# Kernel tuning notes

Measured on AMD Instinct MI355X. Metric: run time of the kernel, lower is better.

The kernel has to match this reference:

```python
import jax, jax.numpy as jnp
import numpy as np
import math

B, C, MX, MY, MZ = 4, 64, 32, 32, 32
N_ATOM, EMB, N_HEAD = 64, 128, 8
HEAD = C // N_HEAD


def setup_inputs() -> dict:
    key = jax.random.key(0)
    ks = jax.random.split(key, 12)
    s = 0.05
    return {
        "x": jax.random.normal(ks[0], (B, C, MX, MY, MZ), jnp.float32),
        "mol_embed": jax.random.normal(ks[1], (B, N_ATOM, EMB), jnp.float32),
        "batch_nodes": jax.random.randint(ks[2], (B,), 1, N_ATOM + 1),  # >=1 valid atom
        "Wq": jax.random.normal(ks[3], (C, C), jnp.float32) * s,
        "bq": jnp.zeros((C,), jnp.float32),
        "Wk": jax.random.normal(ks[4], (C, EMB), jnp.float32) * s,
        "bk": jnp.zeros((C,), jnp.float32),
        "Wv": jax.random.normal(ks[5], (C, EMB), jnp.float32) * s,
        "bv": jnp.zeros((C,), jnp.float32),
        "Wo": jax.random.normal(ks[6], (C, C), jnp.float32) * s,
        "bo": jnp.zeros((C,), jnp.float32),
        "Wc": jax.random.normal(ks[7], (C, C, 3, 3, 3), jnp.float32) * s,
        "bc": jnp.zeros((C,), jnp.float32),
    }


def reference(x, mol_embed, batch_nodes, Wq, bq, Wk, bk, Wv, bv, Wo, bo, Wc, bc):
    b, c, mx, my, mz = x.shape
    m_voxel = mx * my * mz
    n_atom = mol_embed.shape[1]
    x_in = x

    # [b, m_voxel, c] voxel tokens
    xt = x.reshape(b, c, m_voxel).transpose(0, 2, 1)
    q = (xt @ Wq.T + bq).reshape(b, m_voxel, N_HEAD, HEAD)
    k = (mol_embed @ Wk.T + bk).reshape(b, n_atom, N_HEAD, HEAD)
    v = (mol_embed @ Wv.T + bv).reshape(b, n_atom, N_HEAD, HEAD)

    att = jnp.einsum('bqhd,bkhd->bhqk', q, k) / math.sqrt(HEAD)
    # ragged per-batch masking: atoms >= batch_nodes[i] are invalid
    valid = jnp.arange(n_atom)[None, :] < batch_nodes[:, None]  # [b, n_atom]
    att = jnp.where(valid[:, None, None, :], att, -jnp.inf)
    att = jax.nn.softmax(att, axis=-1)

    o = jnp.einsum('bhqk,bkhd->bqhd', att, v).reshape(b, m_voxel, c)
    o = jax.nn.relu(o @ Wo.T + bo)
    o = o.transpose(0, 2, 1).reshape(b, c, mx, my, mz)

    # conv3d k=3 with circular padding
    op = jnp.pad(o, ((0, 0), (0, 0), (1, 1), (1, 1), (1, 1)), mode='wrap')
    conv = jax.lax.conv_general_dilated(
        op, Wc, window_strides=(1, 1, 1), padding='VALID',
        dimension_numbers=('NCDHW', 'OIDHW', 'NCDHW'))
    conv = conv + bc[None, :, None, None, None]
    return jax.nn.relu(conv) + x_in
```

## Files before the change

### kernel.cpp

```cpp
#include <hip/hip_runtime.h>
#include <hip/hip_bf16.h>

#define B_    4
#define C_    64
#define MVOX  32768
#define NATOM 64
#define EMB_  128

typedef __attribute__((ext_vector_type(8)))  __bf16 bf16x8;
typedef __attribute__((ext_vector_type(4)))  float  f32x4;
typedef __attribute__((ext_vector_type(16))) float  f32x16;
typedef __attribute__((ext_vector_type(8)))  unsigned short ushort8;

typedef __attribute__((address_space(1))) const unsigned int gas_u32;
typedef __attribute__((address_space(3))) unsigned int las_u32;

static __device__ __forceinline__ unsigned short bf16u(float f) {
  __hip_bfloat16 h = __float2bfloat16(f);
  return *(unsigned short*)&h;
}

__global__ __launch_bounds__(256) void wprep_kernel(
    const float* __restrict__ Wc, const float* __restrict__ Wq,
    const float* __restrict__ Wo, const float* __restrict__ Wk,
    const float* __restrict__ Wv,
    __hip_bfloat16* __restrict__ Wt4, __hip_bfloat16* __restrict__ Wqb,
    __hip_bfloat16* __restrict__ Wob, __hip_bfloat16* __restrict__ Wkb,
    __hip_bfloat16* __restrict__ Wvb) {
  const int i = blockIdx.x * 256 + threadIdx.x;
  if (i < 110592) {
    const int tap = i >> 12;
    const int coh = (i >> 11) & 1;
    const int ks  = (i >> 9) & 3;
    const int l   = (i >> 3) & 63;
    const int j   = i & 7;
    const int co  = coh * 32 + (l & 31);
    const int ci  = ks * 16 + ((l >> 5) << 3) + j;
    Wt4[i] = __float2bfloat16(Wc[(co * C_ + ci) * 27 + tap]);
  } else if (i < 114688) {
    const int i2 = i - 110592;
    const int nf = (i2 >> 10) & 3;
    const int kk = (i2 >> 9) & 1;
    const int l  = (i2 >> 3) & 63;
    const int j  = i2 & 7;
    const int co = nf * 16 + (l & 15);
    const int ci = kk * 32 + ((l >> 4) << 3) + j;
    Wqb[i2] = __float2bfloat16(Wq[co * C_ + ci] * 0.3535533905932738f);
  } else if (i < 118784) {
    const int i3 = i - 114688;
    const int nf = (i3 >> 10) & 3;
    const int kk = (i3 >> 9) & 1;
    const int l  = (i3 >> 3) & 63;
    const int j  = i3 & 7;
    const int co = nf * 16 + (l & 15);
    const int ci = kk * 32 + ((l >> 4) << 3) + j;
    Wob[i3] = __float2bfloat16(Wo[co * C_ + ci]);
  } else if (i < 135168) {
    const int i4 = (i - 118784) & 8191;
    const bool is_v = (i - 118784) >= 8192;
    const int ch = i4 >> 12;
    const int kk = (i4 >> 9) & 7;
    const int l  = (i4 >> 3) & 63;
    const int j  = i4 & 7;
    const int c  = ch * 32 + (l & 31);
    const int e  = kk * 16 + ((l >> 5) << 3) + j;
    const float v = (is_v ? Wv : Wk)[c * EMB_ + e];
    (is_v ? Wvb : Wkb)[i4] = __float2bfloat16(v);
  }
}

__global__ __launch_bounds__(256) void kv_kernel(
    const float* __restrict__ mol,
    const __hip_bfloat16* __restrict__ Wkb, const float* __restrict__ bk,
    const __hip_bfloat16* __restrict__ Wvb, const float* __restrict__ bv,
    unsigned short* __restrict__ kfb, unsigned short* __restrict__ vfb) {
  __shared__ float smol[NATOM][132];
  __shared__ float res[2][NATOM][68];

  const int b    = blockIdx.x;
  const int tid  = threadIdx.x;
  const int lane = tid & 63;
  const int w    = tid >> 6;
  const int kvw  = w >> 1;
  const int ah   = w & 1;

  for (int i = tid; i < 2048; i += 256) {
    const int a = i >> 4, cb = (i & 15) * 8;
    const f32x4 v0 = *(const f32x4*)&mol[(size_t)(b * NATOM + a) * EMB_ + cb];
    const f32x4 v1 = *(const f32x4*)&mol[(size_t)(b * NATOM + a) * EMB_ + cb + 4];
    *(f32x4*)&smol[a][cb]     = v0;
    *(f32x4*)&smol[a][cb + 4] = v1;
  }
  __syncthreads();

  const __hip_bfloat16* Wb   = kvw ? Wvb : Wkb;
  const float*          bias = kvw ? bv : bk;

  f32x16 acc[2];
  #pragma unroll
  for (int ch = 0; ch < 2; ++ch)
    #pragma unroll
    for (int r = 0; r < 16; ++r) acc[ch][r] = 0.f;

  const int a = ah * 32 + (lane & 31);
  #pragma unroll
  for (int kk = 0; kk < 8; ++kk) {
    const int e0 = kk * 16 + ((lane >> 5) << 3);
    ushort8 au;
    #pragma unroll
    for (int j = 0; j < 8; ++j) au[j] = bf16u(smol[a][e0 + j]);
    const bf16x8 af = __builtin_bit_cast(bf16x8, au);
    #pragma unroll
    for (int ch = 0; ch < 2; ++ch) {
      const bf16x8 bf = *(const bf16x8*)(Wb + (((ch * 8 + kk) << 6) + lane) * 8);
      acc[ch] = __builtin_amdgcn_mfma_f32_32x32x16_bf16(af, bf, acc[ch], 0, 0, 0);
    }
  }

  #pragma unroll
  for (int ch = 0; ch < 2; ++ch) {
    const int c = ch * 32 + (lane & 31);
    const float bb = bias[c];
    #pragma unroll
    for (int r = 0; r < 16; ++r) {
      const int ar = ah * 32 + (r & 3) + 8 * (r >> 2) + 4 * (lane >> 5);
      res[kvw][ar][c] = acc[ch][r] + bb;
    }
  }
  __syncthreads();

  #pragma unroll
  for (int t = 0; t < 8; ++t) {
    const int idx = t * 256 + tid;
    const int h = idx >> 8, aa = (idx >> 6) & 3, ln = idx & 63;
    const int qd = ln >> 4, l15 = ln & 15;
    ushort8 au;
    if (qd == 0) {
      #pragma unroll
      for (int j = 0; j < 8; ++j) au[j] = bf16u(res[0][aa * 16 + l15][h * 8 + j]);
    } else {
      #pragma unroll
      for (int j = 0; j < 8; ++j) au[j] = 0;
    }
    *(ushort8*)(kfb + (size_t)(((b * 8 + h) * 4 + aa) * 64 + ln) * 8) = au;
  }
  #pragma unroll
  for (int t = 0; t < 4; ++t) {
    const int idx = t * 256 + tid;
    const int h = idx >> 7, s = (idx >> 6) & 1, ln = idx & 63;
    const int qd = ln >> 4, l15 = ln & 15;
    ushort8 au;
    #pragma unroll
    for (int j = 0; j < 8; ++j) {
      const int atom = (2 * s + (j >> 2)) * 16 + qd * 4 + (j & 3);
      au[j] = bf16u(res[1][atom][h * 8 + (l15 & 7)]);
    }
    *(ushort8*)(vfb + (size_t)(((b * 8 + h) * 2 + s) * 64 + ln) * 8) = au;
  }
}

__global__ __launch_bounds__(512, 4) void attn_kernel(
    const float* __restrict__ x,
    const unsigned short* __restrict__ kfb, const unsigned short* __restrict__ vfb,
    const int* __restrict__ batch_nodes,
    const __hip_bfloat16* __restrict__ Wqb, const float* __restrict__ bq,
    const __hip_bfloat16* __restrict__ Wob, const float* __restrict__ bo,
    __hip_bfloat16* __restrict__ omid) {
  __shared__ float buf[64 * C_];

  const int b    = blockIdx.y;
  const int m0   = blockIdx.x * 64;
  const int tid  = threadIdx.x;
  const int lane = tid & 63;
  const int w    = __builtin_amdgcn_readfirstlane(tid >> 6);
  const int h    = w;
  const int quad = lane >> 4;
  const int l15  = lane & 15;
  const int vq   = w & 3;
  const int cq   = w >> 2;

  bf16x8 kf[4], vf[2];
  #pragma unroll
  for (int a = 0; a < 4; ++a)
    kf[a] = __builtin_bit_cast(bf16x8,
        *(const ushort8*)(kfb + (size_t)(((b * 8 + h) * 4 + a) * 64 + lane) * 8));
  #pragma unroll
  for (int s = 0; s < 2; ++s)
    vf[s] = __builtin_bit_cast(bf16x8,
        *(const ushort8*)(vfb + (size_t)(((b * 8 + h) * 2 + s) * 64 + lane) * 8));

  #pragma unroll
  for (int j = 0; j < 2; ++j) {
    const int cidx = w * 2 + j;
    const int c  = cidx * 4 + (lane >> 4);
    const int v4 = (lane & 15) * 4;
    const float* gsrc = x + (size_t)(b * C_ + c) * MVOX + m0 + v4;
    __builtin_amdgcn_global_load_lds((gas_u32*)gsrc,
                                     (las_u32*)&buf[cidx * 256], 16, 0, 0);
  }
  __syncthreads();

  f32x4 qacc[2];
  {
    bf16x8 af[2];
    #pragma unroll
    for (int kk = 0; kk < 2; ++kk) {
      ushort8 au;
      #pragma unroll
      for (int j = 0; j < 8; ++j)
        au[j] = bf16u(buf[(kk * 32 + quad * 8 + j) * 64 + vq * 16 + l15]);
      af[kk] = __builtin_bit_cast(bf16x8, au);
    }
    #pragma unroll
    for (int nf2 = 0; nf2 < 2; ++nf2) {
      const int nf = cq * 2 + nf2;
      const float bqv = bq[nf * 16 + l15] * 0.3535533905932738f;
      qacc[nf2] = {bqv, bqv, bqv, bqv};
      #pragma unroll
      for (int kk = 0; kk < 2; ++kk) {
        const bf16x8 bf = *(const bf16x8*)(Wqb + (((nf * 2 + kk) << 6) + lane) * 8);
        qacc[nf2] = __builtin_amdgcn_mfma_f32_16x16x32_bf16(af[kk], bf, qacc[nf2], 0, 0, 0);
      }
    }
  }
  __syncthreads();

  unsigned short* qb = (unsigned short*)buf;
  #pragma unroll
  for (int nf2 = 0; nf2 < 2; ++nf2) {
    const int co = (cq * 2 + nf2) * 16 + l15;
    #pragma unroll
    for (int r = 0; r < 4; ++r) {
      const int vr = vq * 16 + quad * 4 + r;
      qb[vr * 64 + (((co >> 3) ^ (vr & 7)) << 3) + (co & 7)] = bf16u(qacc[nf2][r]);
    }
  }
  __syncthreads();

  const int nv = batch_nodes[b];
  unsigned short* ob = (unsigned short*)buf + 4096;

  f32x4 oacc[4];
  #pragma unroll
  for (int v = 0; v < 4; ++v)
    #pragma unroll
    for (int r = 0; r < 4; ++r) oacc[v][r] = 0.f;

  const f32x4 zero4 = {0.f, 0.f, 0.f, 0.f};
  #pragma unroll
  for (int v = 0; v < 4; ++v) {
    const int qrow = v * 16 + l15;
    const bf16x8 qf = __builtin_bit_cast(bf16x8,
        *(const ushort8*)&qb[qrow * 64 + ((h ^ (qrow & 7)) << 3)]);

    f32x4 st[4];
    #pragma unroll
    for (int a = 0; a < 4; ++a)
      st[a] = __builtin_amdgcn_mfma_f32_16x16x32_bf16(kf[a], qf, zero4, 0, 0, 0);

    float m = -1e30f;
    #pragma unroll
    for (int a = 0; a < 4; ++a)
      #pragma unroll
      for (int r = 0; r < 4; ++r) {
        const int atom = a * 16 + quad * 4 + r;
        const float val = (atom < nv) ? st[a][r] : -1e30f;
        st[a][r] = val;
        m = fmaxf(m, val);
      }
    m = fmaxf(m, __shfl_xor(m, 16, 64));
    m = fmaxf(m, __shfl_xor(m, 32, 64));
    float ssum = 0.f;
    #pragma unroll
    for (int a = 0; a < 4; ++a)
      #pragma unroll
      for (int r = 0; r < 4; ++r) {
        const float p = __expf(st[a][r] - m);
        st[a][r] = p;
        ssum += p;
      }
    ssum += __shfl_xor(ssum, 16, 64);
    ssum += __shfl_xor(ssum, 32, 64);
    const float inv = 1.f / ssum;

    #pragma unroll
    for (int s = 0; s < 2; ++s) {
      ushort8 pu;
      #pragma unroll
      for (int j = 0; j < 8; ++j)
        pu[j] = bf16u(st[2 * s + (j >> 2)][j & 3] * inv);
      const bf16x8 pa = __builtin_bit_cast(bf16x8, pu);
      oacc[v] = __builtin_amdgcn_mfma_f32_16x16x32_bf16(pa, vf[s], oacc[v], 0, 0, 0);
    }
  }

  if (l15 < 8) {
    #pragma unroll
    for (int v = 0; v < 4; ++v)
      #pragma unroll
      for (int r = 0; r < 4; ++r) {
        const int vxr = v * 16 + quad * 4 + r;
        ob[vxr * 64 + ((h ^ (vxr & 7)) << 3) + l15] = bf16u(oacc[v][r]);
      }
  }
  __syncthreads();

  {
    bf16x8 af[2];
    #pragma unroll
    for (int kk = 0; kk < 2; ++kk) {
      const int row = vq * 16 + l15;
      af[kk] = __builtin_bit_cast(bf16x8,
          *(const ushort8*)&ob[row * 64 + (((kk * 4 + quad) ^ (row & 7)) << 3)]);
    }
    f32x4 oac[2];
    #pragma unroll
    for (int nf2 = 0; nf2 < 2; ++nf2) {
      const int nf = cq * 2 + nf2;
      const float bov = bo[nf * 16 + l15];
      oac[nf2] = {bov, bov, bov, bov};
      #pragma unroll
      for (int kk = 0; kk < 2; ++kk) {
        const bf16x8 bf = *(const bf16x8*)(Wob + (((nf * 2 + kk) << 6) + lane) * 8);
        oac[nf2] = __builtin_amdgcn_mfma_f32_16x16x32_bf16(af[kk], bf, oac[nf2], 0, 0, 0);
      }
    }
    __syncthreads();
    unsigned short* osb = (unsigned short*)buf;
    #pragma unroll
    for (int nf2 = 0; nf2 < 2; ++nf2) {
      const int co = (cq * 2 + nf2) * 16 + l15;
      #pragma unroll
      for (int r = 0; r < 4; ++r) {
        const int vr = vq * 16 + quad * 4 + r;
        osb[vr * 64 + (((co >> 3) ^ (vr & 7)) << 3) + (co & 7)] =
            bf16u(fmaxf(oac[nf2][r], 0.f));
      }
    }
  }
  __syncthreads();

  *(ushort8*)(omid + (size_t)(b * MVOX + m0) * C_ + tid * 8) =
      *(const ushort8*)&((unsigned short*)buf)[tid * 8];
}

#define LOADB(dst, DX, DY, DZ)                                              \
  {                                                                         \
    const int zp_ = ((lane & 31) + (DZ) + 31) & 31;                         \
    const int sw_ = zp_ & 7;                                                \
    const int hl_ = (lpx + (DX)) * 4 + (lpy + (DY));                        \
    _Pragma("unroll")                                                       \
    for (int ks_ = 0; ks_ < 4; ++ks_) {                                     \
      const int phys_ = (ks_ * 2 + (lane >> 5)) ^ sw_;                      \
      (dst)[ks_] = *(const bf16x8*)&halo[((hl_ * 32 + zp_) * 8 + phys_) * 8]; \
    }                                                                       \
  }

#define LOADW(T2)                                                           \
  _Pragma("unroll")                                                         \
  for (int f_ = 0; f_ < 8; ++f_)                                            \
    wf[(T2) % 3][f_] = *(const bf16x8*)(                                    \
        Wt4 + ((((T2) * 2 + (f_ >> 2)) * 4 + (f_ & 3)) << 9) + lane * 8);

#define DOMFMA(src, T)                                                      \
  _Pragma("unroll")                                                         \
  for (int ks_ = 0; ks_ < 4; ++ks_)                                         \
    _Pragma("unroll")                                                       \
    for (int ch_ = 0; ch_ < 2; ++ch_)                                       \
      acc[ch_] = __builtin_amdgcn_mfma_f32_32x32x16_bf16(                   \
          wf[(T) % 3][ch_ * 4 + ks_], (src)[ks_], acc[ch_], 0, 0, 0);

__global__ __launch_bounds__(256, 2) void conv_kernel(
    const __hip_bfloat16* __restrict__ omid,
    const __hip_bfloat16* __restrict__ Wt4,
    const float* __restrict__ bc,
    const float* __restrict__ xin,
    float* __restrict__ out) {
  __shared__ __hip_bfloat16 halo[512 * 64];

  const int b    = blockIdx.y;
  const int x0   = (blockIdx.x >> 4) * 2;
  const int y0   = (blockIdx.x & 15) * 2;
  const int tid  = threadIdx.x;
  const int lane = tid & 63;
  const int w    = tid >> 6;
  const int lpx  = w >> 1;
  const int lpy  = w & 1;

  {
    const __hip_bfloat16* src = omid + (size_t)b * MVOX * C_;
    #pragma unroll
    for (int n = 0; n < 16; ++n) {
      const int chunk = w * 16 + n;
      const int li = chunk >> 2;
      const int zb = (chunk & 3) * 8;
      const int gx = (x0 - 1 + (li >> 2)) & 31;
      const int gy = (y0 - 1 + (li & 3)) & 31;
      const __hip_bfloat16* gsrc = src + (size_t)(gx * 1024 + gy * 32 + zb) * C_ + lane * 8;
      __builtin_amdgcn_global_load_lds((gas_u32*)gsrc,
                                       (las_u32*)&halo[chunk * 512], 16, 0, 0);
    }
  }

  bf16x8 wf[3][8];
  LOADW(0);
  LOADW(1);
  __syncthreads();

  f32x16 acc[2];
  #pragma unroll
  for (int i = 0; i < 2; ++i)
    #pragma unroll
    for (int r = 0; r < 16; ++r) acc[i][r] = 0.f;

  bf16x8 bA[4], bB[4];
  LOADB(bA, 0, 0, 0);

  #pragma unroll
  for (int t = 0; t < 27; ++t) {
    const int dxn = (t + 1) / 9, dyn = ((t + 1) / 3) % 3, dzn = (t + 1) % 3;
    if ((t & 1) == 0) {
      if (t < 26) LOADB(bB, dxn, dyn, dzn);
      if (t < 25) LOADW(t + 2);
      DOMFMA(bA, t);
    } else {
      if (t < 26) LOADB(bA, dxn, dyn, dzn);
      if (t < 25) LOADW(t + 2);
      DOMFMA(bB, t);
    }
  }

  const int z = lane & 31;
  const int gx = x0 + lpx, gy = y0 + lpy;
  #pragma unroll
  for (int ch = 0; ch < 2; ++ch) {
    #pragma unroll
    for (int r = 0; r < 16; ++r) {
      const int co = ch * 32 + (r & 3) + 8 * (r >> 2) + 4 * (lane >> 5);
      const size_t idx = ((size_t)(b * C_ + co)) * MVOX + gx * 1024 + gy * 32 + z;
      out[idx] = fmaxf(acc[ch][r] + bc[co], 0.f) + xin[idx];
    }
  }
}

extern "C" void kernel_launch(void* const* d_in, const int* in_sizes, int n_in,
                              void* d_out, int out_size, void* d_ws, size_t ws_size,
                              hipStream_t stream) {
  const float* x   = (const float*)d_in[0];
  const float* mol = (const float*)d_in[1];
  const int*   bn  = (const int*)  d_in[2];
  const float* Wq  = (const float*)d_in[3];
  const float* bq  = (const float*)d_in[4];
  const float* Wk  = (const float*)d_in[5];
  const float* bk  = (const float*)d_in[6];
  const float* Wv  = (const float*)d_in[7];
  const float* bv  = (const float*)d_in[8];
  const float* Wo  = (const float*)d_in[9];
  const float* bo  = (const float*)d_in[10];
  const float* Wc  = (const float*)d_in[11];
  const float* bc  = (const float*)d_in[12];
  float* out = (float*)d_out;

  char* ws = (char*)d_ws;
  __hip_bfloat16* omid = (__hip_bfloat16*)ws;
  __hip_bfloat16* Wt4  = (__hip_bfloat16*)(ws + 16777216);
  __hip_bfloat16* Wqb  = (__hip_bfloat16*)(ws + 16998400);
  __hip_bfloat16* Wob  = (__hip_bfloat16*)(ws + 17006592);
  __hip_bfloat16* Wkb  = (__hip_bfloat16*)(ws + 17014784);
  __hip_bfloat16* Wvb  = (__hip_bfloat16*)(ws + 17031168);
  unsigned short* kfb  = (unsigned short*)(ws + 17047552);
  unsigned short* vfb  = (unsigned short*)(ws + 17178624);

  wprep_kernel<<<dim3(528), 256, 0, stream>>>(Wc, Wq, Wo, Wk, Wv,
                                              Wt4, Wqb, Wob, Wkb, Wvb);
  kv_kernel<<<dim3(B_), 256, 0, stream>>>(mol, Wkb, bk, Wvb, bv, kfb, vfb);
  attn_kernel<<<dim3(MVOX / 64, B_), 512, 0, stream>>>(x, kfb, vfb, bn, Wqb, bq, Wob, bo, omid);
  conv_kernel<<<dim3(256, B_), 256, 0, stream>>>(omid, Wt4, bc, x, out);
}
```

Baseline: 86.26 us.

## Halve conv waves, each computing two x-columns to reuse weight fragments

The conv kernel now launches 128 threads (2 waves) per block instead of 4, and each wave computes outputs for two x positions, keeping four accumulator tiles. Each weight fragment loaded into registers is reused across both x columns, halving per-block weight traffic from global/L2. The cost is much higher register pressure (launch bounds 128,1), fewer waves per block to hide latency, and each wave issuing twice the halo loads.

```diff
diff --git a/kernel.cpp b/kernel.cpp
--- a/kernel.cpp
+++ b/kernel.cpp
@@ -348,11 +348,15 @@
   {                                                                         \
     const int zp_ = ((lane & 31) + (DZ) + 31) & 31;                         \
     const int sw_ = zp_ & 7;                                                \
-    const int hl_ = (lpx + (DX)) * 4 + (lpy + (DY));                        \
     _Pragma("unroll")                                                       \
     for (int ks_ = 0; ks_ < 4; ++ks_) {                                     \
       const int phys_ = (ks_ * 2 + (lane >> 5)) ^ sw_;                      \
-      (dst)[ks_] = *(const bf16x8*)&halo[((hl_ * 32 + zp_) * 8 + phys_) * 8]; \
+      _Pragma("unroll")                                                     \
+      for (int xl_ = 0; xl_ < 2; ++xl_) {                                   \
+        const int hl_ = (xl_ + (DX)) * 4 + (wy + (DY));                     \
+        (dst)[xl_ * 4 + ks_] =                                              \
+            *(const bf16x8*)&halo[((hl_ * 32 + zp_) * 8 + phys_) * 8];      \
+      }                                                                     \
     }                                                                       \
   }
 
@@ -366,11 +370,14 @@
   _Pragma("unroll")                                                         \
   for (int ks_ = 0; ks_ < 4; ++ks_)                                         \
     _Pragma("unroll")                                                       \
-    for (int ch_ = 0; ch_ < 2; ++ch_)                                       \
-      acc[ch_] = __builtin_amdgcn_mfma_f32_32x32x16_bf16(                   \
-          wf[(T) % 3][ch_ * 4 + ks_], (src)[ks_], acc[ch_], 0, 0, 0);
-
-__global__ __launch_bounds__(256, 2) void conv_kernel(
+    for (int xl_ = 0; xl_ < 2; ++xl_)                                       \
+      _Pragma("unroll")                                                     \
+      for (int ch_ = 0; ch_ < 2; ++ch_)                                     \
+        acc[xl_][ch_] = __builtin_amdgcn_mfma_f32_32x32x16_bf16(            \
+            wf[(T) % 3][ch_ * 4 + ks_], (src)[xl_ * 4 + ks_],               \
+            acc[xl_][ch_], 0, 0, 0);
+
+__global__ __launch_bounds__(128, 1) void conv_kernel(
     const __hip_bfloat16* __restrict__ omid,
     const __hip_bfloat16* __restrict__ Wt4,
     const float* __restrict__ bc,
@@ -383,15 +390,13 @@
   const int y0   = (blockIdx.x & 15) * 2;
   const int tid  = threadIdx.x;
   const int lane = tid & 63;
-  const int w    = tid >> 6;
-  const int lpx  = w >> 1;
-  const int lpy  = w & 1;
+  const int wy   = tid >> 6;
 
   {
     const __hip_bfloat16* src = omid + (size_t)b * MVOX * C_;
     #pragma unroll
-    for (int n = 0; n < 16; ++n) {
-      const int chunk = w * 16 + n;
+    for (int n = 0; n < 32; ++n) {
+      const int chunk = wy * 32 + n;
       const int li = chunk >> 2;
       const int zb = (chunk & 3) * 8;
       const int gx = (x0 - 1 + (li >> 2)) & 31;
@@ -407,38 +412,42 @@
   LOADW(1);
   __syncthreads();
 
-  f32x16 acc[2];
-  #pragma unroll
-  for (int i = 0; i < 2; ++i)
-    #pragma unroll
-    for (int r = 0; r < 16; ++r) acc[i][r] = 0.f;
-
-  bf16x8 bA[4], bB[4];
+  f32x16 acc[2][2];
+  #pragma unroll
+  for (int xl = 0; xl < 2; ++xl)
+    #pragma unroll
+    for (int ch = 0; ch < 2; ++ch)
+      #pragma unroll
+      for (int r = 0; r < 16; ++r) acc[xl][ch][r] = 0.f;
+
+  bf16x8 bA[8], bB[8];
   LOADB(bA, 0, 0, 0);
 
   #pragma unroll
   for (int t = 0; t < 27; ++t) {
-    const int dxn = (t + 1) / 9, dyn = ((t + 1) / 3) % 3, dzn = (t + 1) % 3;
-    if ((t & 1) == 0) {
-      if (t < 26) LOADB(bB, dxn, dyn, dzn);
-      if (t < 25) LOADW(t + 2);
-      DOMFMA(bA, t);
-    } else {
-      if (t < 26) LOADB(bA, dxn, dyn, dzn);
-      if (t < 25) LOADW(t + 2);
-      DOMFMA(bB, t);
-    }
+    const int tn = t + 1;
+    if (tn < 27) {
+      if ((t & 1) == 0) LOADB(bB, tn / 9, (tn / 3) % 3, tn % 3)
+      else              LOADB(bA, tn / 9, (tn / 3) % 3, tn % 3)
+    }
+    if (t + 2 < 27) LOADW(t + 2);
+    if ((t & 1) == 0) DOMFMA(bA, t)
+    else              DOMFMA(bB, t)
   }
 
   const int z = lane & 31;
-  const int gx = x0 + lpx, gy = y0 + lpy;
-  #pragma unroll
-  for (int ch = 0; ch < 2; ++ch) {
-    #pragma unroll
-    for (int r = 0; r < 16; ++r) {
-      const int co = ch * 32 + (r & 3) + 8 * (r >> 2) + 4 * (lane >> 5);
-      const size_t idx = ((size_t)(b * C_ + co)) * MVOX + gx * 1024 + gy * 32 + z;
-      out[idx] = fmaxf(acc[ch][r] + bc[co], 0.f) + xin[idx];
+  const int gy = y0 + wy;
+  #pragma unroll
+  for (int xl = 0; xl < 2; ++xl) {
+    const int gx = x0 + xl;
+    #pragma unroll
+    for (int ch = 0; ch < 2; ++ch) {
+      #pragma unroll
+      for (int r = 0; r < 16; ++r) {
+        const int co = ch * 32 + (r & 3) + 8 * (r >> 2) + 4 * (lane >> 5);
+        const size_t idx = ((size_t)(b * C_ + co)) * MVOX + gx * 1024 + gy * 32 + z;
+        out[idx] = fmaxf(acc[xl][ch][r] + bc[co], 0.f) + xin[idx];
+      }
     }
   }
 }
@@ -475,5 +484,5 @@
                                               Wt4, Wqb, Wob, Wkb, Wvb);
   kv_kernel<<<dim3(B_), 256, 0, stream>>>(mol, Wkb, bk, Wvb, bv, kfb, vfb);
   attn_kernel<<<dim3(MVOX / 64, B_), 512, 0, stream>>>(x, kfb, vfb, bn, Wqb, bq, Wob, bo, omid);
-  conv_kernel<<<dim3(256, B_), 256, 0, stream>>>(omid, Wt4, bc, x, out);
-}
+  conv_kernel<<<dim3(256, B_), 128, 0, stream>>>(omid, Wt4, bc, x, out);
+}
```

After: 113.4 us. 31.5% more time.
